# Kernel optimization log

Hardware: AMD Instinct MI355X
Metric: run time of the kernel (lower is better)

Reference implementation:

```python
import jax, jax.numpy as jnp
import numpy as np
from jax.scipy.special import logsumexp

EPS = 0.1
NUM_ITERS = 50
TOPO_MULT = 1.0


def _dist_cosine(x):
    # x: [N, D] -> pairwise cosine distance [N, N], clamped to >= 0
    norms = jnp.sqrt(jnp.clip(jnp.sum(x * x, axis=1, keepdims=True), 1e-8, None))
    xn = x / norms
    return jnp.clip(1.0 - xn @ xn.T, 0.0, None)


def _sinkhorn_log_domain(a, b, C):
    # a, b: [N, N] row-stochastic; C: [N, N]. Duals computed with no grad (detached).
    log_a = jnp.log(jnp.clip(a, 1e-8, None))
    log_b = jnp.log(jnp.clip(b, 1e-8, None))
    la = jax.lax.stop_gradient(log_a)
    lb = jax.lax.stop_gradient(log_b)
    lC = jax.lax.stop_gradient(-C / EPS)[None]  # [1, N, N]

    def body(i, fg):
        f, g = fg
        g = EPS * lb - EPS * logsumexp(f[:, :, None] + lC, axis=1)
        f = EPS * la - EPS * logsumexp(lC + g[:, None, :], axis=2)
        return (f, g)

    f0 = jnp.zeros_like(a)
    f, g = jax.lax.fori_loop(0, NUM_ITERS, body, (f0, f0))
    cost = jnp.sum(a * f, axis=1) + jnp.sum(b * g, axis=1)  # [N]
    return jnp.mean(cost)


def reference(x_original, x_reconstructed, z_latent, log_sigma_lat, log_var_recon, log_var_topo):
    recon_loss = jnp.mean((x_reconstructed - x_original) ** 2)

    D_orig = _dist_cosine(x_original)   # [N, N]
    D_latent = _dist_cosine(z_latent)   # [N, N]

    sigma_orig = jnp.median(D_orig)
    sigma_orig = jnp.where(sigma_orig == 0, jnp.asarray(1e-6, D_orig.dtype), sigma_orig)
    sigma_lat = jax.nn.softplus(log_sigma_lat) + 1e-6  # [1]

    S_orig = jnp.exp(-D_orig ** 2 / (2.0 * sigma_orig ** 2))
    S_lat = jnp.exp(-D_latent ** 2 / (2.0 * sigma_lat ** 2))

    N = S_orig.shape[0]
    mask = 1.0 - jnp.eye(N, dtype=S_orig.dtype)
    S_orig = S_orig * mask
    S_lat = S_lat * mask

    P_orig = S_orig / jnp.clip(jnp.sum(S_orig, axis=1, keepdims=True), 1e-8, None)
    P_lat = S_lat / jnp.clip(jnp.sum(S_lat, axis=1, keepdims=True), 1e-8, None)

    C = D_orig
    ot_orig_lat = _sinkhorn_log_domain(P_orig, P_lat, C)
    ot_lat_lat = _sinkhorn_log_domain(P_lat, P_lat, C)
    ot_orig_orig = _sinkhorn_log_domain(P_orig, P_orig, C)

    topo_loss = jnp.clip(ot_orig_lat - 0.5 * ot_lat_lat - 0.5 * ot_orig_orig, 0.0, None)
    topo_loss = topo_loss * TOPO_MULT

    prec_r = jnp.exp(-log_var_recon)  # [1]
    prec_t = jnp.exp(-log_var_topo)   # [1]
    total_loss = (0.5 * prec_r * recon_loss + 0.5 * log_var_recon
                  + 0.5 * prec_t * topo_loss + 0.5 * log_var_topo)  # [1]
    return (total_loss, recon_loss, topo_loss)


def setup_inputs() -> dict:
    key = jax.random.key(0)
    k1, k2, k3 = jax.random.split(key, 3)
    N, D, DL = 256, 4096, 256
    return {
        "x_original": jax.random.normal(k1, (N, D), dtype=jnp.float32),
        "x_reconstructed": jax.random.normal(k2, (N, D), dtype=jnp.float32),
        "z_latent": jax.random.normal(k3, (N, DL), dtype=jnp.float32),
        "log_sigma_lat": jnp.zeros((1,), dtype=jnp.float32),
        "log_var_recon": jnp.zeros((1,), dtype=jnp.float32),
        "log_var_topo": jnp.zeros((1,), dtype=jnp.float32),
    }
```

## Files before the change

### kernel.cpp

```cpp
#include <hip/hip_runtime.h>
#include <hip/hip_fp16.h>

#define EPS 0.1f
#define SINK_ITERS 50
#define KSCALE_LN 9.0109133472f
#define USTRIDE 264

typedef _Float16 f16;
typedef _Float16 f16x8 __attribute__((ext_vector_type(8)));
typedef float f32x4 __attribute__((ext_vector_type(4)));

#define PIN_U4(v) asm volatile("" : "+v"(v.x), "+v"(v.y), "+v"(v.z), "+v"(v.w))

__device__ __forceinline__ float wave_red_sum(float v) {
    #pragma unroll
    for (int o = 32; o; o >>= 1) v += __shfl_xor(v, o, 64);
    return v;
}

__global__ __launch_bounds__(256) void k_pre(const float4* __restrict__ xo,
                                             const float4* __restrict__ xr,
                                             const float4* __restrict__ z,
                                             float4* __restrict__ xn,
                                             float4* __restrict__ zn,
                                             float* __restrict__ acc) {
    __shared__ float red[4];
    int b = blockIdx.x, t = threadIdx.x;
    if (b < 512) {
        int tid = b * 256 + t;
        float s = 0.f;
        for (int i = tid; i < 262144; i += 512 * 256) {
            float4 a = xo[i], r = xr[i];
            float d0 = r.x - a.x, d1 = r.y - a.y, d2 = r.z - a.z, d3 = r.w - a.w;
            s = fmaf(d0, d0, s); s = fmaf(d1, d1, s);
            s = fmaf(d2, d2, s); s = fmaf(d3, d3, s);
        }
        s = wave_red_sum(s);
        if ((t & 63) == 0) red[t >> 6] = s;
        __syncthreads();
        if (t == 0) atomicAdd(acc + 3, red[0] + red[1] + red[2] + red[3]);
    } else {
        int row = b - 512;
        const float4* src; float4* dst; int c4;
        if (row < 256) { src = xo + (size_t)row * 1024; dst = xn + (size_t)row * 1024; c4 = 1024; }
        else { src = z + (size_t)(row - 256) * 64; dst = zn + (size_t)(row - 256) * 64; c4 = 64; }
        float s = 0.f;
        for (int i = t; i < c4; i += 256) {
            float4 v = src[i];
            s = fmaf(v.x, v.x, s); s = fmaf(v.y, v.y, s);
            s = fmaf(v.z, v.z, s); s = fmaf(v.w, v.w, s);
        }
        s = wave_red_sum(s);
        if ((t & 63) == 0) red[t >> 6] = s;
        __syncthreads();
        float tot = red[0] + red[1] + red[2] + red[3];
        float rn = 1.f / sqrtf(fmaxf(tot, 1e-8f));
        for (int i = t; i < c4; i += 256) {
            float4 v = src[i];
            v.x *= rn; v.y *= rn; v.z *= rn; v.w *= rn;
            dst[i] = v;
        }
    }
}

__global__ __launch_bounds__(256) void k_gemm_aat(const float* __restrict__ xn,
                                                  const float* __restrict__ zn,
                                                  float* __restrict__ part,
                                                  float* __restrict__ part2) {
    __shared__ float At[64][17], Bt[64][17];
    int zb = blockIdx.z;
    const float* A; int lda, k0, nk; float* out;
    if (zb < 16) { A = xn; lda = 4096; k0 = zb * 256; nk = 256; out = part + (size_t)zb * 65536; }
    else { A = zn; lda = 256; k0 = (zb - 16) * 64; nk = 64; out = part2 + (size_t)(zb - 16) * 65536; }
    int i0 = blockIdx.x * 64, j0 = blockIdx.y * 64;
    int t = threadIdx.x, tx = t & 15, ty = t >> 4;
    float acc[4][4] = {};
    for (int kc = 0; kc < nk; kc += 16) {
        __syncthreads();
        #pragma unroll
        for (int m = 0; m < 4; m++) {
            int idx = m * 256 + t;
            int kk = idx & 15, row = idx >> 4;
            At[row][kk] = A[(size_t)(i0 + row) * lda + k0 + kc + kk];
            Bt[row][kk] = A[(size_t)(j0 + row) * lda + k0 + kc + kk];
        }
        __syncthreads();
        #pragma unroll
        for (int kk = 0; kk < 16; kk++) {
            float a[4], b[4];
            #pragma unroll
            for (int m = 0; m < 4; m++) a[m] = At[ty * 4 + m][kk];
            #pragma unroll
            for (int n = 0; n < 4; n++) b[n] = Bt[tx * 4 + n][kk];
            #pragma unroll
            for (int m = 0; m < 4; m++)
                #pragma unroll
                for (int n = 0; n < 4; n++)
                    acc[m][n] = fmaf(a[m], b[n], acc[m][n]);
        }
    }
    #pragma unroll
    for (int m = 0; m < 4; m++) {
        float4 v = make_float4(acc[m][0], acc[m][1], acc[m][2], acc[m][3]);
        *(float4*)&out[(i0 + ty * 4 + m) * 256 + j0 + tx * 4] = v;
    }
}

__global__ __launch_bounds__(256) void k_reduce_do(const float* __restrict__ part,
                                                   float* __restrict__ Do) {
    int e = blockIdx.x * 256 + threadIdx.x;
    float s = 0.f;
    for (int sl = 0; sl < 16; sl++) s += part[(size_t)sl * 65536 + e];
    Do[e] = fmaxf(1.f - s, 0.f);
}

__device__ __forceinline__ int med_bin(float v) {
    int b = (int)(v * 4096.f);
    if (v < (float)b * (1.f / 4096.f)) b--;
    else if (v >= (float)(b + 1) * (1.f / 4096.f)) b++;
    if (b < 0) b = 0;
    if (b > 8191) b = 8191;
    return b;
}

__global__ __launch_bounds__(1024) void k_median(const float* __restrict__ D,
                                                 float* __restrict__ out_sigma) {
    __shared__ int hist[8192];
    __shared__ int redc[16];
    __shared__ int sh_bin[2];
    __shared__ int sh_tot;
    int t = threadIdx.x;
    unsigned r[64];
    #pragma unroll
    for (int i = 0; i < 64; i++) r[i] = __float_as_uint(D[t + i * 1024]);
    #pragma unroll
    for (int j = 0; j < 8; j++) hist[t + j * 1024] = 0;
    __syncthreads();
    #pragma unroll
    for (int i = 0; i < 64; i++)
        atomicAdd(&hist[med_bin(__uint_as_float(r[i]))], 1);
    __syncthreads();
    int s8 = 0;
    #pragma unroll
    for (int j = 0; j < 8; j++) s8 += hist[t * 8 + j];
    int inc = s8;
    #pragma unroll
    for (int o = 1; o < 64; o <<= 1) {
        int vv = __shfl_up(inc, o, 64);
        if ((t & 63) >= o) inc += vv;
    }
    if ((t & 63) == 63) redc[t >> 6] = inc;
    __syncthreads();
    int woff = 0;
    for (int wv = 0; wv < (t >> 6); wv++) woff += redc[wv];
    int excl = woff + inc - s8;
    for (int sel = 0; sel < 2; sel++) {
        int k = 32767 + sel;
        if (excl <= k && k < excl + s8) {
            int cum = excl, bfound = 8191;
            bool found = false;
            for (int j = 0; j < 8; j++) {
                int hc = hist[t * 8 + j];
                if (!found) {
                    if (cum + hc > k) { bfound = t * 8 + j; found = true; }
                    else cum += hc;
                }
            }
            sh_bin[sel] = bfound;
        }
    }
    __syncthreads();
    unsigned res[2];
    for (int sel = 0; sel < 2; sel++) {
        int k = 32767 + sel;
        int b = sh_bin[sel];
        unsigned lo = __float_as_uint((float)b * (1.f / 4096.f));
        unsigned hi = __float_as_uint((float)(b + 1) * (1.f / 4096.f));
        while (hi - lo > 1u) {
            unsigned mid = (lo + hi) >> 1;
            int c = 0;
            #pragma unroll
            for (int i = 0; i < 64; i++) c += (r[i] < mid) ? 1 : 0;
            #pragma unroll
            for (int o = 32; o; o >>= 1) c += __shfl_xor(c, o, 64);
            if ((t & 63) == 0) redc[t >> 6] = c;
            __syncthreads();
            if (t == 0) {
                int tot = 0;
                for (int wv = 0; wv < 16; wv++) tot += redc[wv];
                sh_tot = tot;
            }
            __syncthreads();
            if (sh_tot <= k) lo = mid; else hi = mid;
        }
        res[sel] = lo;
    }
    if (t == 0)
        out_sigma[0] = 0.5f * (__uint_as_float(res[0]) + __uint_as_float(res[1]));
}

__global__ __launch_bounds__(256) void k_prep(const float* __restrict__ Do,
                                              const float* __restrict__ part2,
                                              const float* __restrict__ wsacc,
                                              const float* __restrict__ lsl,
                                              float* __restrict__ Po, float* __restrict__ Pl,
                                              float* __restrict__ ELo, float* __restrict__ ELl,
                                              f16* __restrict__ Kh) {
    __shared__ float red[8];
    int i = blockIdx.x, j = threadIdx.x;
    int e = i * 256 + j;
    float sig_o = wsacc[4];
    if (sig_o == 0.f) sig_o = 1e-6f;
    float x = lsl[0];
    float sp = (x > 20.f) ? x : log1pf(__expf(x));
    float sig_l = sp + 1e-6f;
    float i2o = 1.f / (2.f * sig_o * sig_o);
    float i2l = 1.f / (2.f * sig_l * sig_l);
    float d_o = Do[e];
    float sD = part2[e] + part2[65536 + e] + part2[131072 + e] + part2[196608 + e];
    float d_l = fmaxf(1.f - sD, 0.f);
    float so = (i == j) ? 0.f : __expf(-d_o * d_o * i2o);
    float sl = (i == j) ? 0.f : __expf(-d_l * d_l * i2l);
    float wso = wave_red_sum(so);
    float wsl = wave_red_sum(sl);
    if ((j & 63) == 0) { red[j >> 6] = wso; red[4 + (j >> 6)] = wsl; }
    __syncthreads();
    float sum_o = red[0] + red[1] + red[2] + red[3];
    float sum_l = red[4] + red[5] + red[6] + red[7];
    float po = so / fmaxf(sum_o, 1e-8f);
    float pl = sl / fmaxf(sum_l, 1e-8f);
    Po[e] = po;
    Pl[e] = pl;
    ELo[e] = EPS * __logf(fmaxf(po, 1e-8f));
    ELl[e] = EPS * __logf(fmaxf(pl, 1e-8f));
    float kv = __expf(-d_o * (1.f / EPS) + KSCALE_LN);
    Kh[(((i >> 3) * 256 + j) << 3) + (i & 7)] = (f16)kv;
}

__global__ __launch_bounds__(512, 2) void k_sinkhorn(const float* __restrict__ Po,
                                                     const float* __restrict__ Pl,
                                                     const float* __restrict__ ELo,
                                                     const float* __restrict__ ELl,
                                                     const uint4* __restrict__ Kq,
                                                     float* __restrict__ wsacc) {
    __shared__ __align__(16) f16 U[2][16 * USTRIDE];
    __shared__ float CW[8][16];
    int t = threadIdx.x;
    int lane = t & 63, wv = t >> 6;
    int m16 = lane & 15, quad = lane >> 4;
    int w = blockIdx.x;
    int s = w >> 4;
    int ibase = (w & 15) * 16;

    uint4 bf0[8], bf1[8];
    int cA = 32 * wv + m16, cB = cA + 16;
    #pragma unroll
    for (int kc = 0; kc < 8; kc++) {
        bf0[kc] = Kq[(kc * 4 + quad) * 256 + cA];
        bf1[kc] = Kq[(kc * 4 + quad) * 256 + cB];
    }
    #pragma unroll
    for (int kc = 0; kc < 8; kc++) { PIN_U4(bf0[kc]); PIN_U4(bf1[kc]); }

    const float* ELa_b = (s == 1 ? ELl : ELo);
    const float* ELb_b = (s == 2 ? ELo : ELl);
    float ela[2][4], elb[2][4];
    #pragma unroll
    for (int reg = 0; reg < 4; reg++) {
        int i = ibase + quad * 4 + reg;
        ela[0][reg] = ELa_b[i * 256 + cA] + EPS * KSCALE_LN;
        ela[1][reg] = ELa_b[i * 256 + cB] + EPS * KSCALE_LN;
        elb[0][reg] = ELb_b[i * 256 + cA] + EPS * KSCALE_LN;
        elb[1][reg] = ELb_b[i * 256 + cB] + EPS * KSCALE_LN;
    }

    {
        int row = t >> 5, c0 = (t & 31) * 8;
        *(uint4*)&U[0][row * USTRIDE + c0] =
            make_uint4(0x3C003C00u, 0x3C003C00u, 0x3C003C00u, 0x3C003C00u);
    }
    __syncthreads();

    float df[2][4], dg[2][4];
    #pragma unroll
    for (int reg = 0; reg < 4; reg++) { df[0][reg] = df[1][reg] = dg[0][reg] = dg[1][reg] = 0.f; }

    for (int it = 0; it < 2 * SINK_ITERS; it++) {
        const f16* ub = &U[it & 1][0];
        f16* un = &U[(it + 1) & 1][0];
        f32x4 acc0 = {0.f, 0.f, 0.f, 0.f}, acc1 = {0.f, 0.f, 0.f, 0.f};
        #pragma unroll
        for (int kc = 0; kc < 8; kc++) {
            f16x8 a = *(const f16x8*)&ub[m16 * USTRIDE + kc * 32 + quad * 8];
            acc0 = __builtin_amdgcn_mfma_f32_16x16x32_f16(a, __builtin_bit_cast(f16x8, bf0[kc]),
                                                          acc0, 0, 0, 0);
            acc1 = __builtin_amdgcn_mfma_f32_16x16x32_f16(a, __builtin_bit_cast(f16x8, bf1[kc]),
                                                          acc1, 0, 0, 0);
        }
        bool fstep = (it & 1);
        #pragma unroll
        for (int reg = 0; reg < 4; reg++) {
            int p = quad * 4 + reg;
            float z0 = acc0[reg], z1 = acc1[reg];
            float e0 = fstep ? ela[0][reg] : elb[0][reg];
            float e1 = fstep ? ela[1][reg] : elb[1][reg];
            float d0 = e0 - EPS * __logf(z0);
            float d1 = e1 - EPS * __logf(z1);
            if (fstep) { df[0][reg] = d0; df[1][reg] = d1; }
            else       { dg[0][reg] = d0; dg[1][reg] = d1; }
            un[p * USTRIDE + cA] = (f16)__expf(d0);
            un[p * USTRIDE + cB] = (f16)__expf(d1);
        }
        __syncthreads();
    }

    const float* PaB = (s == 1 ? Pl : Po);
    const float* PbB = (s == 2 ? Po : Pl);
    float cs[4];
    #pragma unroll
    for (int reg = 0; reg < 4; reg++) {
        int i = ibase + quad * 4 + reg;
        cs[reg] = PaB[i * 256 + cA] * df[0][reg] + PbB[i * 256 + cA] * dg[0][reg] +
                  PaB[i * 256 + cB] * df[1][reg] + PbB[i * 256 + cB] * dg[1][reg];
    }
    #pragma unroll
    for (int o = 1; o < 16; o <<= 1) {
        #pragma unroll
        for (int reg = 0; reg < 4; reg++) cs[reg] += __shfl_xor(cs[reg], o, 64);
    }
    if (m16 == 0) {
        #pragma unroll
        for (int reg = 0; reg < 4; reg++) CW[wv][quad * 4 + reg] = cs[reg];
    }
    __syncthreads();
    if (wv == 0) {
        float v = 0.f;
        if (lane < 16) {
            #pragma unroll
            for (int w2 = 0; w2 < 8; w2++) v += CW[w2][lane];
        }
        v = wave_red_sum(v);
        if (lane == 0) atomicAdd(&wsacc[s], v);
    }
}

__global__ void k_final(const float* __restrict__ wsacc, const float* __restrict__ lvr_p,
                        const float* __restrict__ lvt_p, float* __restrict__ out) {
    float recon = wsacc[3] * (1.f / (256.f * 4096.f));
    float ot0 = wsacc[0] * (1.f / 256.f);
    float ot1 = wsacc[1] * (1.f / 256.f);
    float ot2 = wsacc[2] * (1.f / 256.f);
    float topo = ot0 - 0.5f * ot1 - 0.5f * ot2;
    topo = topo > 0.f ? topo : 0.f;
    float lvr = lvr_p[0], lvt = lvt_p[0];
    out[0] = 0.5f * __expf(-lvr) * recon + 0.5f * lvr +
             0.5f * __expf(-lvt) * topo + 0.5f * lvt;
    out[1] = recon;
    out[2] = topo;
}

extern "C" void kernel_launch(void* const* d_in, const int* in_sizes, int n_in,
                              void* d_out, int out_size, void* d_ws, size_t ws_size,
                              hipStream_t stream) {
    const float* xo = (const float*)d_in[0];
    const float* xr = (const float*)d_in[1];
    const float* z  = (const float*)d_in[2];
    const float* lsl = (const float*)d_in[3];
    const float* lvr = (const float*)d_in[4];
    const float* lvt = (const float*)d_in[5];
    float* out = (float*)d_out;
    float* ws = (float*)d_ws;

    float* acc = ws;
    float* xn  = ws + 64;
    float* zn  = xn + 1048576;
    float* Do  = zn + 65536;
    float* Po  = Do + 65536;
    float* Pl  = Po + 65536;
    float* ELo = Pl + 65536;
    float* ELl = ELo + 65536;
    float* Kh  = ELl + 65536;
    float* part = Kh + 32768;
    float* part2 = Po;

    hipMemsetAsync(acc, 0, 64, stream);
    k_pre<<<1024, 256, 0, stream>>>((const float4*)xo, (const float4*)xr, (const float4*)z,
                                    (float4*)xn, (float4*)zn, acc);
    k_gemm_aat<<<dim3(4, 4, 20), 256, 0, stream>>>(xn, zn, part, part2);
    k_reduce_do<<<256, 256, 0, stream>>>(part, Do);
    k_median<<<1, 1024, 0, stream>>>(Do, acc + 4);
    k_prep<<<256, 256, 0, stream>>>(Do, part2, acc, lsl, Po, Pl, ELo, ELl, (f16*)Kh);
    k_sinkhorn<<<48, 512, 0, stream>>>(Po, Pl, ELo, ELl, (const uint4*)Kh, acc);
    k_final<<<1, 1, 0, stream>>>(acc, lvr, lvt, out);
}
```

Baseline: 241.3 us.

## Use fp16 MFMA for cosine Gram and spread Sinkhorn rows across more blocks

Normalized inputs are now stored as fp16, and the Gram matrix is computed with 16x16x32 f16 MFMA instructions instead of scalar fp32 FMAs. The Sinkhorn kernel now gives each block 4 rows instead of 16 and launches 192 blocks instead of 48, so more compute units run the serial iteration loop. Only quad 0 does the log/exp update, and the MFMA A-operand replicates the 4 rows, so three quarters of the MFMA output is wasted. Rounding the normalized features to fp16 lowers the precision of the cosine distances that feed the median and the cost matrix.

```diff
diff --git a/kernel.cpp b/kernel.cpp
--- a/kernel.cpp
+++ b/kernel.cpp
@@ -4,9 +4,10 @@
 #define EPS 0.1f
 #define SINK_ITERS 50
 #define KSCALE_LN 9.0109133472f
-#define USTRIDE 264
+#define USTRIDE 272
 
 typedef _Float16 f16;
+typedef _Float16 f16x4 __attribute__((ext_vector_type(4)));
 typedef _Float16 f16x8 __attribute__((ext_vector_type(8)));
 typedef float f32x4 __attribute__((ext_vector_type(4)));
 
@@ -21,8 +22,8 @@
 __global__ __launch_bounds__(256) void k_pre(const float4* __restrict__ xo,
                                              const float4* __restrict__ xr,
                                              const float4* __restrict__ z,
-                                             float4* __restrict__ xn,
-                                             float4* __restrict__ zn,
+                                             f16x4* __restrict__ xh,
+                                             f16x4* __restrict__ zh,
                                              float* __restrict__ acc) {
     __shared__ float red[4];
     int b = blockIdx.x, t = threadIdx.x;
@@ -41,9 +42,9 @@
         if (t == 0) atomicAdd(acc + 3, red[0] + red[1] + red[2] + red[3]);
     } else {
         int row = b - 512;
-        const float4* src; float4* dst; int c4;
-        if (row < 256) { src = xo + (size_t)row * 1024; dst = xn + (size_t)row * 1024; c4 = 1024; }
-        else { src = z + (size_t)(row - 256) * 64; dst = zn + (size_t)(row - 256) * 64; c4 = 64; }
+        const float4* src; f16x4* dst; int c4;
+        if (row < 256) { src = xo + (size_t)row * 1024; dst = xh + (size_t)row * 1024; c4 = 1024; }
+        else { src = z + (size_t)(row - 256) * 64; dst = zh + (size_t)(row - 256) * 64; c4 = 64; }
         float s = 0.f;
         for (int i = t; i < c4; i += 256) {
             float4 v = src[i];
@@ -57,53 +58,48 @@
         float rn = 1.f / sqrtf(fmaxf(tot, 1e-8f));
         for (int i = t; i < c4; i += 256) {
             float4 v = src[i];
-            v.x *= rn; v.y *= rn; v.z *= rn; v.w *= rn;
-            dst[i] = v;
-        }
-    }
-}
-
-__global__ __launch_bounds__(256) void k_gemm_aat(const float* __restrict__ xn,
-                                                  const float* __restrict__ zn,
+            f16x4 h;
+            h[0] = (f16)(v.x * rn); h[1] = (f16)(v.y * rn);
+            h[2] = (f16)(v.z * rn); h[3] = (f16)(v.w * rn);
+            dst[i] = h;
+        }
+    }
+}
+
+__global__ __launch_bounds__(256) void k_gemm_f16(const uint4* __restrict__ xh,
+                                                  const uint4* __restrict__ zh,
                                                   float* __restrict__ part,
                                                   float* __restrict__ part2) {
-    __shared__ float At[64][17], Bt[64][17];
+    __shared__ __align__(16) f16 Ai[64 * 40], Bj[64 * 40];
     int zb = blockIdx.z;
-    const float* A; int lda, k0, nk; float* out;
-    if (zb < 16) { A = xn; lda = 4096; k0 = zb * 256; nk = 256; out = part + (size_t)zb * 65536; }
-    else { A = zn; lda = 256; k0 = (zb - 16) * 64; nk = 64; out = part2 + (size_t)(zb - 16) * 65536; }
+    const uint4* X; int lda8, k0, nchunk; float* out;
+    if (zb < 16) { X = xh; lda8 = 512; k0 = zb * 256; nchunk = 8; out = part + (size_t)zb * 65536; }
+    else { X = zh; lda8 = 32; k0 = (zb - 16) * 64; nchunk = 2; out = part2 + (size_t)(zb - 16) * 65536; }
     int i0 = blockIdx.x * 64, j0 = blockIdx.y * 64;
-    int t = threadIdx.x, tx = t & 15, ty = t >> 4;
-    float acc[4][4] = {};
-    for (int kc = 0; kc < nk; kc += 16) {
-        __syncthreads();
-        #pragma unroll
-        for (int m = 0; m < 4; m++) {
-            int idx = m * 256 + t;
-            int kk = idx & 15, row = idx >> 4;
-            At[row][kk] = A[(size_t)(i0 + row) * lda + k0 + kc + kk];
-            Bt[row][kk] = A[(size_t)(j0 + row) * lda + k0 + kc + kk];
-        }
-        __syncthreads();
-        #pragma unroll
-        for (int kk = 0; kk < 16; kk++) {
-            float a[4], b[4];
-            #pragma unroll
-            for (int m = 0; m < 4; m++) a[m] = At[ty * 4 + m][kk];
-            #pragma unroll
-            for (int n = 0; n < 4; n++) b[n] = Bt[tx * 4 + n][kk];
-            #pragma unroll
-            for (int m = 0; m < 4; m++)
-                #pragma unroll
-                for (int n = 0; n < 4; n++)
-                    acc[m][n] = fmaf(a[m], b[n], acc[m][n]);
-        }
-    }
-    #pragma unroll
-    for (int m = 0; m < 4; m++) {
-        float4 v = make_float4(acc[m][0], acc[m][1], acc[m][2], acc[m][3]);
-        *(float4*)&out[(i0 + ty * 4 + m) * 256 + j0 + tx * 4] = v;
-    }
+    int t = threadIdx.x, lane = t & 63, wv = t >> 6;
+    int m16 = lane & 15, quad = lane >> 4;
+    int r = t >> 2, ko = (t & 3) * 8;
+    f32x4 acc[4] = {};
+    for (int ch = 0; ch < nchunk; ch++) {
+        int kb8 = (k0 + ch * 32) >> 3;
+        uint4 va = X[(size_t)(i0 + r) * lda8 + kb8 + (t & 3)];
+        uint4 vb = X[(size_t)(j0 + r) * lda8 + kb8 + (t & 3)];
+        __syncthreads();
+        *(uint4*)&Ai[r * 40 + ko] = va;
+        *(uint4*)&Bj[r * 40 + ko] = vb;
+        __syncthreads();
+        f16x8 a = *(const f16x8*)&Ai[(wv * 16 + m16) * 40 + quad * 8];
+        #pragma unroll
+        for (int st = 0; st < 4; st++) {
+            f16x8 bfr = *(const f16x8*)&Bj[(st * 16 + m16) * 40 + quad * 8];
+            acc[st] = __builtin_amdgcn_mfma_f32_16x16x32_f16(a, bfr, acc[st], 0, 0, 0);
+        }
+    }
+    #pragma unroll
+    for (int st = 0; st < 4; st++)
+        #pragma unroll
+        for (int reg = 0; reg < 4; reg++)
+            out[(i0 + wv * 16 + quad * 4 + reg) * 256 + j0 + st * 16 + m16] = acc[st][reg];
 }
 
 __global__ __launch_bounds__(256) void k_reduce_do(const float* __restrict__ part,
@@ -243,14 +239,14 @@
                                                      const float* __restrict__ ELl,
                                                      const uint4* __restrict__ Kq,
                                                      float* __restrict__ wsacc) {
-    __shared__ __align__(16) f16 U[2][16 * USTRIDE];
-    __shared__ float CW[8][16];
+    __shared__ __align__(16) f16 U[2][4 * USTRIDE];
+    __shared__ float CW[8][4];
     int t = threadIdx.x;
     int lane = t & 63, wv = t >> 6;
     int m16 = lane & 15, quad = lane >> 4;
     int w = blockIdx.x;
-    int s = w >> 4;
-    int ibase = (w & 15) * 16;
+    int s = w >> 6;
+    int ibase = (w & 63) * 4;
 
     uint4 bf0[8], bf1[8];
     int cA = 32 * wv + m16, cB = cA + 16;
@@ -264,83 +260,80 @@
 
     const float* ELa_b = (s == 1 ? ELl : ELo);
     const float* ELb_b = (s == 2 ? ELo : ELl);
-    float ela[2][4], elb[2][4];
-    #pragma unroll
-    for (int reg = 0; reg < 4; reg++) {
-        int i = ibase + quad * 4 + reg;
-        ela[0][reg] = ELa_b[i * 256 + cA] + EPS * KSCALE_LN;
-        ela[1][reg] = ELa_b[i * 256 + cB] + EPS * KSCALE_LN;
-        elb[0][reg] = ELb_b[i * 256 + cA] + EPS * KSCALE_LN;
-        elb[1][reg] = ELb_b[i * 256 + cB] + EPS * KSCALE_LN;
-    }
-
-    {
-        int row = t >> 5, c0 = (t & 31) * 8;
-        *(uint4*)&U[0][row * USTRIDE + c0] =
+    float ela[2][4] = {}, elb[2][4] = {};
+    if (quad == 0) {
+        #pragma unroll
+        for (int reg = 0; reg < 4; reg++) {
+            int i = ibase + reg;
+            ela[0][reg] = ELa_b[i * 256 + cA] + EPS * KSCALE_LN;
+            ela[1][reg] = ELa_b[i * 256 + cB] + EPS * KSCALE_LN;
+            elb[0][reg] = ELb_b[i * 256 + cA] + EPS * KSCALE_LN;
+            elb[1][reg] = ELb_b[i * 256 + cB] + EPS * KSCALE_LN;
+        }
+    }
+
+    if (t < 136)
+        *(uint4*)&U[0][t * 8] =
             make_uint4(0x3C003C00u, 0x3C003C00u, 0x3C003C00u, 0x3C003C00u);
-    }
-    __syncthreads();
-
-    float df[2][4], dg[2][4];
-    #pragma unroll
-    for (int reg = 0; reg < 4; reg++) { df[0][reg] = df[1][reg] = dg[0][reg] = dg[1][reg] = 0.f; }
-
+    __syncthreads();
+
+    float df[2][4] = {}, dg[2][4] = {};
     for (int it = 0; it < 2 * SINK_ITERS; it++) {
         const f16* ub = &U[it & 1][0];
         f16* un = &U[(it + 1) & 1][0];
         f32x4 acc0 = {0.f, 0.f, 0.f, 0.f}, acc1 = {0.f, 0.f, 0.f, 0.f};
         #pragma unroll
         for (int kc = 0; kc < 8; kc++) {
-            f16x8 a = *(const f16x8*)&ub[m16 * USTRIDE + kc * 32 + quad * 8];
+            f16x8 a = *(const f16x8*)&ub[(m16 & 3) * USTRIDE + kc * 32 + quad * 8];
             acc0 = __builtin_amdgcn_mfma_f32_16x16x32_f16(a, __builtin_bit_cast(f16x8, bf0[kc]),
                                                           acc0, 0, 0, 0);
             acc1 = __builtin_amdgcn_mfma_f32_16x16x32_f16(a, __builtin_bit_cast(f16x8, bf1[kc]),
                                                           acc1, 0, 0, 0);
         }
         bool fstep = (it & 1);
-        #pragma unroll
-        for (int reg = 0; reg < 4; reg++) {
-            int p = quad * 4 + reg;
-            float z0 = acc0[reg], z1 = acc1[reg];
-            float e0 = fstep ? ela[0][reg] : elb[0][reg];
-            float e1 = fstep ? ela[1][reg] : elb[1][reg];
-            float d0 = e0 - EPS * __logf(z0);
-            float d1 = e1 - EPS * __logf(z1);
-            if (fstep) { df[0][reg] = d0; df[1][reg] = d1; }
-            else       { dg[0][reg] = d0; dg[1][reg] = d1; }
-            un[p * USTRIDE + cA] = (f16)__expf(d0);
-            un[p * USTRIDE + cB] = (f16)__expf(d1);
+        if (quad == 0) {
+            #pragma unroll
+            for (int reg = 0; reg < 4; reg++) {
+                float z0 = acc0[reg], z1 = acc1[reg];
+                float e0 = fstep ? ela[0][reg] : elb[0][reg];
+                float e1 = fstep ? ela[1][reg] : elb[1][reg];
+                float d0 = e0 - EPS * __logf(z0);
+                float d1 = e1 - EPS * __logf(z1);
+                if (fstep) { df[0][reg] = d0; df[1][reg] = d1; }
+                else       { dg[0][reg] = d0; dg[1][reg] = d1; }
+                un[reg * USTRIDE + cA] = (f16)__expf(d0);
+                un[reg * USTRIDE + cB] = (f16)__expf(d1);
+            }
         }
         __syncthreads();
     }
 
     const float* PaB = (s == 1 ? Pl : Po);
     const float* PbB = (s == 2 ? Po : Pl);
-    float cs[4];
-    #pragma unroll
-    for (int reg = 0; reg < 4; reg++) {
-        int i = ibase + quad * 4 + reg;
-        cs[reg] = PaB[i * 256 + cA] * df[0][reg] + PbB[i * 256 + cA] * dg[0][reg] +
-                  PaB[i * 256 + cB] * df[1][reg] + PbB[i * 256 + cB] * dg[1][reg];
+    float cs[4] = {};
+    if (quad == 0) {
+        #pragma unroll
+        for (int reg = 0; reg < 4; reg++) {
+            int i = ibase + reg;
+            cs[reg] = PaB[i * 256 + cA] * df[0][reg] + PbB[i * 256 + cA] * dg[0][reg] +
+                      PaB[i * 256 + cB] * df[1][reg] + PbB[i * 256 + cB] * dg[1][reg];
+        }
     }
     #pragma unroll
     for (int o = 1; o < 16; o <<= 1) {
         #pragma unroll
         for (int reg = 0; reg < 4; reg++) cs[reg] += __shfl_xor(cs[reg], o, 64);
     }
-    if (m16 == 0) {
-        #pragma unroll
-        for (int reg = 0; reg < 4; reg++) CW[wv][quad * 4 + reg] = cs[reg];
-    }
-    __syncthreads();
-    if (wv == 0) {
+    if (lane == 0) {
+        #pragma unroll
+        for (int reg = 0; reg < 4; reg++) CW[wv][reg] = cs[reg];
+    }
+    __syncthreads();
+    if (t == 0) {
         float v = 0.f;
-        if (lane < 16) {
-            #pragma unroll
-            for (int w2 = 0; w2 < 8; w2++) v += CW[w2][lane];
-        }
-        v = wave_red_sum(v);
-        if (lane == 0) atomicAdd(&wsacc[s], v);
+        for (int w2 = 0; w2 < 8; w2++)
+            v += CW[w2][0] + CW[w2][1] + CW[w2][2] + CW[w2][3];
+        atomicAdd(&wsacc[s], v);
     }
 }
 
@@ -372,9 +365,9 @@
     float* ws = (float*)d_ws;
 
     float* acc = ws;
-    float* xn  = ws + 64;
-    float* zn  = xn + 1048576;
-    float* Do  = zn + 65536;
+    float* xh  = ws + 64;
+    float* zh  = xh + 524288;
+    float* Do  = zh + 32768;
     float* Po  = Do + 65536;
     float* Pl  = Po + 65536;
     float* ELo = Pl + 65536;
@@ -385,11 +378,12 @@
 
     hipMemsetAsync(acc, 0, 64, stream);
     k_pre<<<1024, 256, 0, stream>>>((const float4*)xo, (const float4*)xr, (const float4*)z,
-                                    (float4*)xn, (float4*)zn, acc);
-    k_gemm_aat<<<dim3(4, 4, 20), 256, 0, stream>>>(xn, zn, part, part2);
+                                    (f16x4*)xh, (f16x4*)zh, acc);
+    k_gemm_f16<<<dim3(4, 4, 20), 256, 0, stream>>>((const uint4*)xh, (const uint4*)zh,
+                                                   part, part2);
     k_reduce_do<<<256, 256, 0, stream>>>(part, Do);
     k_median<<<1, 1024, 0, stream>>>(Do, acc + 4);
     k_prep<<<256, 256, 0, stream>>>(Do, part2, acc, lsl, Po, Pl, ELo, ELl, (f16*)Kh);
-    k_sinkhorn<<<48, 512, 0, stream>>>(Po, Pl, ELo, ELl, (const uint4*)Kh, acc);
+    k_sinkhorn<<<192, 512, 0, stream>>>(Po, Pl, ELo, ELl, (const uint4*)Kh, acc);
     k_final<<<1, 1, 0, stream>>>(acc, lvr, lvt, out);
 }
```

After: 223.1 us. 7.5% less time.
